# Kernel tuning notes

Hardware: AMD Instinct MI355X
Metric: run time of the kernel (lower is better)

## Reference

```python
import jax, jax.numpy as jnp
import numpy as np

ALPHA = 0.2  # LeakyReLU negative slope
NEG_INF = -1000000000.0


def setup_inputs() -> dict:
    key = jax.random.key(0)
    k1, k2, k3, k4 = jax.random.split(key, 4)
    B, N, F_in, F_out = 8, 2048, 128, 64
    h = jax.random.normal(k1, (B, N, F_in), dtype=jnp.float32)
    adj_mask = jax.random.randint(k2, (N, N), 0, 2, dtype=jnp.int32)
    # params of nn.Linear(in,out,bias=False) stored as (in,out) for x@W
    W = jax.random.normal(k3, (F_in, F_out), dtype=jnp.float32) * (1.0 / np.sqrt(F_in))
    # attention vector a of nn.Linear(2*out, 1, bias=False) -> shape (2*out,)
    a = jax.random.normal(k4, (2 * F_out,), dtype=jnp.float32) * (1.0 / np.sqrt(2 * F_out))
    return {"h": h, "adj_mask": adj_mask, "W": W, "a": a}


def reference(h, adj_mask, W, a):
    # h: (B,N,Fin), adj_mask: (N,N), W: (Fin,Fout), a: (2*Fout,)
    F_out = a.shape[0] // 2
    h_prime = jnp.einsum('bni,io->bno', h, W)            # (B,N,Fout)
    # a @ concat(h_i, h_j) == a_l @ h_i + a_r @ h_j  (avoids O(B*N*N*2F) concat)
    a_l, a_r = a[:F_out], a[F_out:]
    e_l = h_prime @ a_l                                  # (B,N) score for row node i
    e_r = h_prime @ a_r                                  # (B,N) score for col node j
    e = jax.nn.leaky_relu(e_l[:, :, None] + e_r[:, None, :], negative_slope=ALPHA)  # (B,N,N)
    scores = jnp.where(adj_mask[None, :, :] > 0, e, NEG_INF)
    attention = jax.nn.softmax(scores, axis=-1)          # (B,N,N)
    # dropout is identity in eval mode (training=False)
    h_output = jnp.einsum('bij,bjo->bio', attention, h_prime)  # (B,N,Fout)
    return h_output, attention
```

## Files before the change

kernel.cpp:

```cpp
#include <hip/hip_runtime.h>
#include <hip/hip_bf16.h>

#define B_ 8
#define N_ 2048
#define FIN_ 128
#define FO_ 64
#define ALPHA_ 0.2f
#define NEGINF_ -1000000000.0f

typedef __attribute__((ext_vector_type(8))) short short8;
typedef __attribute__((ext_vector_type(4))) float f32x4;

__device__ __forceinline__ unsigned bf16_rne(float x) {
    union { float f; unsigned u; } v; v.f = x;
    return (v.u + 0x7FFFu + ((v.u >> 16) & 1u)) >> 16;
}
__device__ __forceinline__ float bf16_f32(unsigned b) {
    union { unsigned u; float f; } v; v.u = b << 16; return v.f;
}
__device__ __forceinline__ void split2(float x0, float x1, unsigned& hw, unsigned& lw) {
    unsigned h0 = bf16_rne(x0), h1 = bf16_rne(x1);
    unsigned l0 = bf16_rne(x0 - bf16_f32(h0));
    unsigned l1 = bf16_rne(x1 - bf16_f32(h1));
    hw = h0 | (h1 << 16);
    lw = l0 | (l1 << 16);
}

__global__ __launch_bounds__(256) void k0_bits(
    const int* __restrict__ adj, unsigned* __restrict__ bits)
{
    int i = blockIdx.x, tid = threadIdx.x, lane = tid & 63;
#pragma unroll
    for (int c = 0; c < 8; ++c) {
        int j = c * 256 + tid;
        unsigned long long m = __ballot(adj[(size_t)i * N_ + j] > 0);
        if (lane == 0) {
            bits[(size_t)i * 64 + (j >> 5)]     = (unsigned)m;
            bits[(size_t)i * 64 + (j >> 5) + 1] = (unsigned)(m >> 32);
        }
    }
}

__global__ __launch_bounds__(256) void k1_hprime(
    const float* __restrict__ h, const float* __restrict__ W,
    const float* __restrict__ a,
    unsigned short* __restrict__ hpTh, unsigned short* __restrict__ hpTl,
    float* __restrict__ el, float* __restrict__ er)
{
    __shared__ float Wl[FIN_ * FO_];
    __shared__ float al[FO_], ar[FO_];
    __shared__ float hrow[4][4][FIN_];
    __shared__ float tr[FO_][17];

    int tid = threadIdx.x;
    const float4* W4 = (const float4*)W;
    float4* Wl4 = (float4*)Wl;
#pragma unroll
    for (int i = 0; i < 8; ++i) Wl4[tid + 256 * i] = W4[tid + 256 * i];
    if (tid < FO_) { al[tid] = a[tid]; ar[tid] = a[FO_ + tid]; }

    int wave = tid >> 6, lane = tid & 63;
    int row0 = blockIdx.x * 16 + wave * 4;
#pragma unroll
    for (int rr = 0; rr < 4; ++rr) {
        hrow[wave][rr][lane]      = h[(size_t)(row0 + rr) * FIN_ + lane];
        hrow[wave][rr][lane + 64] = h[(size_t)(row0 + rr) * FIN_ + lane + 64];
    }
    __syncthreads();

    float acc0 = 0.f, acc1 = 0.f, acc2 = 0.f, acc3 = 0.f;
#pragma unroll 8
    for (int k = 0; k < FIN_; ++k) {
        float w = Wl[k * FO_ + lane];
        acc0 = fmaf(hrow[wave][0][k], w, acc0);
        acc1 = fmaf(hrow[wave][1][k], w, acc1);
        acc2 = fmaf(hrow[wave][2][k], w, acc2);
        acc3 = fmaf(hrow[wave][3][k], w, acc3);
    }

    float accs[4] = {acc0, acc1, acc2, acc3};
#pragma unroll
    for (int rr = 0; rr < 4; ++rr) {
        int row = row0 + rr;
        tr[lane][wave * 4 + rr] = accs[rr];
        float pl = accs[rr] * al[lane];
        float pr = accs[rr] * ar[lane];
#pragma unroll
        for (int off = 32; off; off >>= 1) {
            pl += __shfl_xor(pl, off);
            pr += __shfl_xor(pr, off);
        }
        if (lane == 0) { el[row] = pl; er[row] = pr; }
    }
    __syncthreads();

    int o = tid >> 2, kq = tid & 3;
    int gk0 = (blockIdx.x * 16) & (N_ - 1);
    int bb  = (blockIdx.x * 16) >> 11;
    float x0 = tr[o][kq * 4 + 0], x1 = tr[o][kq * 4 + 1];
    float x2 = tr[o][kq * 4 + 2], x3 = tr[o][kq * 4 + 3];
    unsigned hw0, lw0, hw1, lw1;
    split2(x0, x1, hw0, lw0);
    split2(x2, x3, hw1, lw1);
    size_t base = ((size_t)bb * FO_ + o) * N_ + gk0 + kq * 4;
    uint2 H = {hw0, hw1}, L = {lw0, lw1};
    *(uint2*)&hpTh[base] = H;
    *(uint2*)&hpTl[base] = L;
}

__global__ __launch_bounds__(256, 4) void k23_fused(
    const unsigned* __restrict__ bits, const float* __restrict__ el,
    const float* __restrict__ er,
    const unsigned short* __restrict__ hpTh, const unsigned short* __restrict__ hpTl,
    float* __restrict__ attn, float* __restrict__ hout)
{
    __shared__ alignas(16) float erb[N_];
    __shared__ unsigned adjw[16 * 65];
    __shared__ float el16[16], inv16[16];
    __shared__ alignas(16) unsigned short Pt[4][16][40];
    __shared__ alignas(16) unsigned short Pl[4][16][40];
    __shared__ float red[4][16][FO_];

    int tid = threadIdx.x;
    int wave = tid >> 6, lane = tid & 63;
    int i0 = blockIdx.x * 16;
    int b  = blockIdx.y;

    const float4* erg = (const float4*)(er + (size_t)b * N_);
    float4* erb4 = (float4*)erb;
    erb4[tid]       = erg[tid];
    erb4[tid + 256] = erg[tid + 256];
#pragma unroll
    for (int q = 0; q < 4; ++q) {
        int idx = q * 256 + tid;
        adjw[(idx >> 6) * 65 + (idx & 63)] =
            bits[(size_t)(i0 + (idx >> 6)) * 64 + (idx & 63)];
    }
    if (tid < 16) el16[tid] = el[(size_t)b * N_ + i0 + tid];
    __syncthreads();

    const float LOG2E = 1.44269504088896340736f;

    float4 ercache[8];
#pragma unroll
    for (int c = 0; c < 8; ++c) ercache[c] = erb4[c * 64 + lane];

#pragma unroll
    for (int rr = 0; rr < 4; ++rr) {
        int r = wave * 4 + rr;
        float elv = el16[r];
        float sum = 0.f;
#pragma unroll
        for (int c = 0; c < 8; ++c) {
            unsigned w = adjw[r * 65 + c * 8 + (lane >> 3)];
            int b0 = (lane & 7) * 4;
            float xs[4] = {ercache[c].x, ercache[c].y, ercache[c].z, ercache[c].w};
#pragma unroll
            for (int q = 0; q < 4; ++q) {
                float x = elv + xs[q];
                x = fmaxf(x, ALPHA_ * x);
                x = ((w >> (b0 + q)) & 1u) ? x : NEGINF_;
                sum += __builtin_amdgcn_exp2f(x * LOG2E);
            }
        }
#pragma unroll
        for (int off = 32; off; off >>= 1) sum += __shfl_xor(sum, off);
        if (lane == 0) inv16[r] = 1.0f / sum;
    }
    __syncthreads();

    int l15 = lane & 15, lg = lane >> 4;
    int prow = lane >> 2;
    int pj4  = lane & 3;
    float pel  = el16[prow];
    float pinv = inv16[prow];
    int kbase = wave * (N_ / 4);

    float* attnb = attn + (size_t)b * N_ * N_;
    const unsigned short* Bh = hpTh + (size_t)b * FO_ * N_;
    const unsigned short* Bl = hpTl + (size_t)b * FO_ * N_;
    unsigned short* PtW = &Pt[wave][0][0];
    unsigned short* PlW = &Pl[wave][0][0];

    f32x4 acc[4];
#pragma unroll
    for (int c = 0; c < 4; ++c) acc[c] = (f32x4){0.f, 0.f, 0.f, 0.f};

#pragma unroll 1
    for (int ks = kbase; ks < kbase + N_ / 4; ks += 32) {
        short8 bhi[4], blo[4];
#pragma unroll
        for (int c = 0; c < 4; ++c) {
            size_t boff = (size_t)(c * 16 + l15) * N_ + ks + lg * 8;
            bhi[c] = *(const short8*)&Bh[boff];
            blo[c] = *(const short8*)&Bl[boff];
        }

        float4 e0 = erb4[(ks >> 2) + pj4];
        float4 e1 = erb4[(ks >> 2) + 4 + pj4];
        unsigned mw = adjw[prow * 65 + (ks >> 5)];
        int bq = pj4 * 4;
        float e0a[4] = {e0.x, e0.y, e0.z, e0.w};
        float e1a[4] = {e1.x, e1.y, e1.z, e1.w};
        float p0[4], p1[4];
#pragma unroll
        for (int q = 0; q < 4; ++q) {
            float x = pel + e0a[q];
            x = fmaxf(x, ALPHA_ * x);
            x = ((mw >> (bq + q)) & 1u) ? x : NEGINF_;
            p0[q] = __builtin_amdgcn_exp2f(x * LOG2E) * pinv;
            float y = pel + e1a[q];
            y = fmaxf(y, ALPHA_ * y);
            y = ((mw >> (16 + bq + q)) & 1u) ? y : NEGINF_;
            p1[q] = __builtin_amdgcn_exp2f(y * LOG2E) * pinv;
        }

        size_t arow = (size_t)(i0 + prow) * N_ + ks;
        float4 s0 = {p0[0], p0[1], p0[2], p0[3]};
        float4 s1 = {p1[0], p1[1], p1[2], p1[3]};
        *(float4*)&attnb[arow + bq]      = s0;
        *(float4*)&attnb[arow + 16 + bq] = s1;

        unsigned hw0, lw0, hw1, lw1, hw2, lw2, hw3, lw3;
        split2(p0[0], p0[1], hw0, lw0); split2(p0[2], p0[3], hw1, lw1);
        split2(p1[0], p1[1], hw2, lw2); split2(p1[2], p1[3], hw3, lw3);
        uint2 H0 = {hw0, hw1}, H1 = {hw2, hw3}, L0 = {lw0, lw1}, L1 = {lw2, lw3};
        *(uint2*)&PtW[prow * 40 + bq]      = H0;
        *(uint2*)&PtW[prow * 40 + 16 + bq] = H1;
        *(uint2*)&PlW[prow * 40 + bq]      = L0;
        *(uint2*)&PlW[prow * 40 + 16 + bq] = L1;

        short8 ahi = *(const short8*)&PtW[l15 * 40 + lg * 8];
        short8 alo = *(const short8*)&PlW[l15 * 40 + lg * 8];

#pragma unroll
        for (int c = 0; c < 4; ++c) {
            acc[c] = __builtin_amdgcn_mfma_f32_16x16x32_bf16(ahi, bhi[c], acc[c], 0, 0, 0);
            acc[c] = __builtin_amdgcn_mfma_f32_16x16x32_bf16(ahi, blo[c], acc[c], 0, 0, 0);
            acc[c] = __builtin_amdgcn_mfma_f32_16x16x32_bf16(alo, bhi[c], acc[c], 0, 0, 0);
        }
    }

#pragma unroll
    for (int c = 0; c < 4; ++c)
#pragma unroll
        for (int r = 0; r < 4; ++r)
            red[wave][lg * 4 + r][c * 16 + l15] = acc[c][r];
    __syncthreads();

    int oo = tid & 63;
    int ib = tid >> 6;
#pragma unroll
    for (int q = 0; q < 4; ++q) {
        int i = ib * 4 + q;
        float s = (red[0][i][oo] + red[1][i][oo]) + (red[2][i][oo] + red[3][i][oo]);
        hout[((size_t)b * N_ + i0 + i) * FO_ + oo] = s;
    }
}

extern "C" void kernel_launch(void* const* d_in, const int* in_sizes, int n_in,
                              void* d_out, int out_size, void* d_ws, size_t ws_size,
                              hipStream_t stream) {
    const float* h   = (const float*)d_in[0];
    const int*   adj = (const int*)d_in[1];
    const float* W   = (const float*)d_in[2];
    const float* a   = (const float*)d_in[3];

    float* hout = (float*)d_out;
    float* attn = (float*)d_out + (size_t)B_ * N_ * FO_;

    const size_t hpN = (size_t)B_ * FO_ * N_;
    unsigned short* hpTh = (unsigned short*)d_ws;
    unsigned short* hpTl = hpTh + hpN;
    float* elw = (float*)(hpTl + hpN);
    float* erw = elw + (size_t)B_ * N_;
    unsigned* bits = (unsigned*)(erw + (size_t)B_ * N_);

    k0_bits<<<N_, 256, 0, stream>>>(adj, bits);
    k1_hprime<<<(B_ * N_) / 16, 256, 0, stream>>>(h, W, a, hpTh, hpTl, elw, erw);
    k23_fused<<<dim3(N_ / 16, B_), 256, 0, stream>>>(bits, elw, erw, hpTh, hpTl, attn, hout);
}
```

Measured before the change: 222.3 us.

## Compute attention probabilities directly in MFMA A-operand layout, drop LDS staging

Each lane now computes the eight softmax probabilities that match its slot in the MFMA A operand (row l15, columns lg*8..+7). It converts them to bf16 hi/lo pairs in registers, so the per-wave LDS transpose buffers and their write/read round trip go away. The grid is also reordered so batch is the fast block index, which groups blocks sharing the same adjacency rows. The trade-off is that attention stores become two float4 per lane across 16 rows, which is less coalesced than before.

```diff
diff --git a/kernel.cpp b/kernel.cpp
--- a/kernel.cpp
+++ b/kernel.cpp
@@ -117,14 +117,12 @@
     __shared__ alignas(16) float erb[N_];
     __shared__ unsigned adjw[16 * 65];
     __shared__ float el16[16], inv16[16];
-    __shared__ alignas(16) unsigned short Pt[4][16][40];
-    __shared__ alignas(16) unsigned short Pl[4][16][40];
     __shared__ float red[4][16][FO_];
 
     int tid = threadIdx.x;
     int wave = tid >> 6, lane = tid & 63;
-    int i0 = blockIdx.x * 16;
-    int b  = blockIdx.y;
+    int b  = blockIdx.x;
+    int i0 = blockIdx.y * 16;
 
     const float4* erg = (const float4*)(er + (size_t)b * N_);
     float4* erb4 = (float4*)erb;
@@ -170,17 +168,14 @@
     __syncthreads();
 
     int l15 = lane & 15, lg = lane >> 4;
-    int prow = lane >> 2;
-    int pj4  = lane & 3;
-    float pel  = el16[prow];
-    float pinv = inv16[prow];
+    float pel  = el16[l15];
+    float pinv = inv16[l15];
     int kbase = wave * (N_ / 4);
-
-    float* attnb = attn + (size_t)b * N_ * N_;
+    unsigned mrow = l15 * 65;
+
+    float* arow = attn + (size_t)b * N_ * N_ + (size_t)(i0 + l15) * N_ + lg * 8;
     const unsigned short* Bh = hpTh + (size_t)b * FO_ * N_;
     const unsigned short* Bl = hpTl + (size_t)b * FO_ * N_;
-    unsigned short* PtW = &Pt[wave][0][0];
-    unsigned short* PlW = &Pl[wave][0][0];
 
     f32x4 acc[4];
 #pragma unroll
@@ -196,42 +191,33 @@
             blo[c] = *(const short8*)&Bl[boff];
         }
 
-        float4 e0 = erb4[(ks >> 2) + pj4];
-        float4 e1 = erb4[(ks >> 2) + 4 + pj4];
-        unsigned mw = adjw[prow * 65 + (ks >> 5)];
-        int bq = pj4 * 4;
-        float e0a[4] = {e0.x, e0.y, e0.z, e0.w};
-        float e1a[4] = {e1.x, e1.y, e1.z, e1.w};
-        float p0[4], p1[4];
-#pragma unroll
-        for (int q = 0; q < 4; ++q) {
-            float x = pel + e0a[q];
+        int j0 = ks + lg * 8;
+        float4 e0 = erb4[(j0 >> 2)];
+        float4 e1 = erb4[(j0 >> 2) + 1];
+        unsigned mw = adjw[mrow + (ks >> 5)];
+        int bq = lg * 8;
+        float ea[8] = {e0.x, e0.y, e0.z, e0.w, e1.x, e1.y, e1.z, e1.w};
+        float p[8];
+#pragma unroll
+        for (int q = 0; q < 8; ++q) {
+            float x = pel + ea[q];
             x = fmaxf(x, ALPHA_ * x);
             x = ((mw >> (bq + q)) & 1u) ? x : NEGINF_;
-            p0[q] = __builtin_amdgcn_exp2f(x * LOG2E) * pinv;
-            float y = pel + e1a[q];
-            y = fmaxf(y, ALPHA_ * y);
-            y = ((mw >> (16 + bq + q)) & 1u) ? y : NEGINF_;
-            p1[q] = __builtin_amdgcn_exp2f(y * LOG2E) * pinv;
-        }
-
-        size_t arow = (size_t)(i0 + prow) * N_ + ks;
-        float4 s0 = {p0[0], p0[1], p0[2], p0[3]};
-        float4 s1 = {p1[0], p1[1], p1[2], p1[3]};
-        *(float4*)&attnb[arow + bq]      = s0;
-        *(float4*)&attnb[arow + 16 + bq] = s1;
-
-        unsigned hw0, lw0, hw1, lw1, hw2, lw2, hw3, lw3;
-        split2(p0[0], p0[1], hw0, lw0); split2(p0[2], p0[3], hw1, lw1);
-        split2(p1[0], p1[1], hw2, lw2); split2(p1[2], p1[3], hw3, lw3);
-        uint2 H0 = {hw0, hw1}, H1 = {hw2, hw3}, L0 = {lw0, lw1}, L1 = {lw2, lw3};
-        *(uint2*)&PtW[prow * 40 + bq]      = H0;
-        *(uint2*)&PtW[prow * 40 + 16 + bq] = H1;
-        *(uint2*)&PlW[prow * 40 + bq]      = L0;
-        *(uint2*)&PlW[prow * 40 + 16 + bq] = L1;
-
-        short8 ahi = *(const short8*)&PtW[l15 * 40 + lg * 8];
-        short8 alo = *(const short8*)&PlW[l15 * 40 + lg * 8];
+            p[q] = __builtin_amdgcn_exp2f(x * LOG2E) * pinv;
+        }
+
+        float4 s0 = {p[0], p[1], p[2], p[3]};
+        float4 s1 = {p[4], p[5], p[6], p[7]};
+        *(float4*)&arow[ks]     = s0;
+        *(float4*)&arow[ks + 4] = s1;
+
+        short8 ahi, alo;
+#pragma unroll
+        for (int q = 0; q < 8; ++q) {
+            unsigned hb = bf16_rne(p[q]);
+            ahi[q] = (short)hb;
+            alo[q] = (short)bf16_rne(p[q] - bf16_f32(hb));
+        }
 
 #pragma unroll
         for (int c = 0; c < 4; ++c) {
@@ -278,5 +264,5 @@
 
     k0_bits<<<N_, 256, 0, stream>>>(adj, bits);
     k1_hprime<<<(B_ * N_) / 16, 256, 0, stream>>>(h, W, a, hpTh, hpTl, elw, erw);
-    k23_fused<<<dim3(N_ / 16, B_), 256, 0, stream>>>(bits, elw, erw, hpTh, hpTl, attn, hout);
-}
+    k23_fused<<<dim3(B_, N_ / 16), 256, 0, stream>>>(bits, elw, erw, hpTh, hpTl, attn, hout);
+}
```

Measured after the change: 223.4 us. About the same (+0.5%).
